# Kernel optimization log

Hardware: AMD Instinct MI355X
Metric: run time of the kernel (lower is better)

## Reference

```python
import jax, jax.numpy as jnp
import numpy as np
from jax import lax

BETA = 0.9
SLOPE = 25.0
THRESHOLD = 1.0
TIME_STEPS = 50


@jax.custom_vjp
def spike_fn(mem):
    # Heaviside fire: spk = 1 if mem > threshold
    return (mem > THRESHOLD).astype(mem.dtype)

def _spike_fwd(mem):
    return spike_fn(mem), mem

def _spike_bwd(mem, g):
    # snntorch fast_sigmoid surrogate: grad = 1 / (slope*|mem - thr| + 1)^2
    denom = SLOPE * jnp.abs(mem - THRESHOLD) + 1.0
    return (g / (denom * denom),)

spike_fn.defvjp(_spike_fwd, _spike_bwd)


def setup_inputs() -> dict:
    key = jax.random.key(0)
    k = jax.random.split(key, 5)
    B, D, H, O = 16384, 784, 128, 10
    return {
        "data": jax.random.normal(k[0], (B, D), dtype=jnp.float32),
        "W1": jax.random.normal(k[1], (H, D), dtype=jnp.float32) * (1.0 / np.sqrt(D)),
        "b1": jax.random.normal(k[2], (H,), dtype=jnp.float32) * 0.01,
        "W2": jax.random.normal(k[3], (O, H), dtype=jnp.float32) * (1.0 / np.sqrt(H)),
        "b2": jax.random.normal(k[4], (O,), dtype=jnp.float32) * 0.01,
    }


def reference(data, W1, b1, W2, b2):
    B = data.shape[0]
    H, O = W1.shape[0], W2.shape[0]
    # Input current to layer 1 is constant across time steps (static image).
    cur1 = data @ W1.T + b1  # [B, H]

    def step(carry, _):
        mem1, mem2 = carry
        # snntorch Leaky (reset_mechanism='subtract'):
        #   reset = detach(spk(mem_t)); mem_{t+1} = beta*mem_t + I - reset*thr; spk = fire(mem_{t+1})
        rst1 = lax.stop_gradient((mem1 > THRESHOLD).astype(mem1.dtype))
        mem1 = BETA * mem1 + cur1 - rst1 * THRESHOLD
        spk1 = spike_fn(mem1)

        cur2 = spk1 @ W2.T + b2  # [B, O]
        rst2 = lax.stop_gradient((mem2 > THRESHOLD).astype(mem2.dtype))
        mem2 = BETA * mem2 + cur2 - rst2 * THRESHOLD
        spk2 = spike_fn(mem2)
        return (mem1, mem2), spk2

    init = (jnp.zeros((B, H), data.dtype), jnp.zeros((B, O), data.dtype))
    _, spk_rec = lax.scan(step, init, None, length=TIME_STEPS)
    return spk_rec  # [time_steps, B, 10]
```

## Files before the change

kernel.cpp:

```cpp
#include <hip/hip_runtime.h>


#define TSTEPS 50
#define NB 16384
#define ND 784
#define NH 128
#define NO 10

#define BK 16
#define LDT 68

__global__ __launch_bounds__(256, 2)
void gemm_cur1(const float* __restrict__ data, const float* __restrict__ W1,
               const float* __restrict__ b1, float* __restrict__ cur1)
{
    __shared__ float As[BK * LDT];
    __shared__ float Ws[BK * LDT];

    const int tid  = threadIdx.x;
    const int bx   = blockIdx.x;
    const int bm   = bx >> 1;
    const int bn   = bx & 1;
    const int row0 = bm * 64;
    const int col0 = bn * 64;

    const int lm = tid >> 2;
    const int lk = (tid & 3) * 4;

    const float* aSrc = data + (size_t)(row0 + lm) * ND + lk;
    const float* wSrc = W1   + (size_t)(col0 + lm) * ND + lk;

    const int tx = tid & 15;
    const int ty = tid >> 4;

    float4 aReg = *(const float4*)aSrc;
    float4 wReg = *(const float4*)wSrc;

    float acc[4][4] = {};

    for (int c = 0; c < 49; ++c) {
        __syncthreads();
        As[(lk + 0) * LDT + lm] = aReg.x;
        As[(lk + 1) * LDT + lm] = aReg.y;
        As[(lk + 2) * LDT + lm] = aReg.z;
        As[(lk + 3) * LDT + lm] = aReg.w;
        Ws[(lk + 0) * LDT + lm] = wReg.x;
        Ws[(lk + 1) * LDT + lm] = wReg.y;
        Ws[(lk + 2) * LDT + lm] = wReg.z;
        Ws[(lk + 3) * LDT + lm] = wReg.w;
        __syncthreads();
        if (c < 48) {
            aReg = *(const float4*)(aSrc + (c + 1) * BK);
            wReg = *(const float4*)(wSrc + (c + 1) * BK);
        }
        #pragma unroll
        for (int k = 0; k < BK; ++k) {
            float4 a4 = *(const float4*)&As[k * LDT + ty * 4];
            float4 b4 = *(const float4*)&Ws[k * LDT + tx * 4];
            float av[4] = {a4.x, a4.y, a4.z, a4.w};
            float bv[4] = {b4.x, b4.y, b4.z, b4.w};
            #pragma unroll
            for (int i = 0; i < 4; ++i)
                #pragma unroll
                for (int j = 0; j < 4; ++j)
                    acc[i][j] = fmaf(av[i], bv[j], acc[i][j]);
        }
    }

    float4 bv1 = *(const float4*)&b1[col0 + tx * 4];
    #pragma unroll
    for (int i = 0; i < 4; ++i) {
        float4 o;
        o.x = acc[i][0] + bv1.x;
        o.y = acc[i][1] + bv1.y;
        o.z = acc[i][2] + bv1.z;
        o.w = acc[i][3] + bv1.w;
        *(float4*)&cur1[(size_t)(row0 + ty * 4 + i) * NH + col0 + tx * 4] = o;
    }
}

__global__ void snn_loop(const float* __restrict__ cur1,
                         const float* __restrict__ W2,
                         const float* __restrict__ b2,
                         float* __restrict__ out)
{
    const int tid = threadIdx.x;
    const int hg  = tid & 15;
    const int rl  = tid >> 4;
    const int row = blockIdx.x * 16 + rl;
    const int h0  = hg * 8;

    float w2[10][8];
    #pragma unroll
    for (int o = 0; o < 10; ++o) {
        float4 u = *(const float4*)&W2[o * NH + h0];
        float4 v = *(const float4*)&W2[o * NH + h0 + 4];
        w2[o][0] = u.x; w2[o][1] = u.y; w2[o][2] = u.z; w2[o][3] = u.w;
        w2[o][4] = v.x; w2[o][5] = v.y; w2[o][6] = v.z; w2[o][7] = v.w;
    }
    const float b2r = b2[hg < 10 ? hg : 0];

    float c[8];
    {
        float4 c0 = *(const float4*)&cur1[(size_t)row * NH + h0];
        float4 c1 = *(const float4*)&cur1[(size_t)row * NH + h0 + 4];
        c[0] = c0.x; c[1] = c0.y; c[2] = c0.z; c[3] = c0.w;
        c[4] = c1.x; c[5] = c1.y; c[6] = c1.z; c[7] = c1.w;
    }

    float mem1[8], spk1[8];
    #pragma unroll
    for (int j = 0; j < 8; ++j) { mem1[j] = 0.f; spk1[j] = 0.f; }
    float mem2 = 0.f, spk2 = 0.f;

    for (int t = 0; t < TSTEPS; ++t) {
        #pragma unroll
        for (int j = 0; j < 8; ++j) {
            float m = __fadd_rn(__fmul_rn(0.9f, mem1[j]), c[j]);
            m = __fsub_rn(m, spk1[j]);
            mem1[j] = m;
            spk1[j] = (m > 1.0f) ? 1.0f : 0.0f;
        }
        float p[10];
        #pragma unroll
        for (int o = 0; o < 10; ++o) p[o] = 0.f;
        #pragma unroll
        for (int j = 0; j < 8; ++j)
            #pragma unroll
            for (int o = 0; o < 10; ++o)
                p[o] = fmaf(spk1[j], w2[o][j], p[o]);
        #pragma unroll
        for (int m = 1; m <= 8; m <<= 1)
            #pragma unroll
            for (int o = 0; o < 10; ++o)
                p[o] += __shfl_xor(p[o], m, 64);
        float tot = p[0];
        #pragma unroll
        for (int o = 1; o < 10; ++o)
            tot = (hg == o) ? p[o] : tot;
        float cur2 = __fadd_rn(tot, b2r);
        float m2 = __fsub_rn(__fadd_rn(__fmul_rn(0.9f, mem2), cur2), spk2);
        mem2 = m2;
        spk2 = (m2 > 1.0f) ? 1.0f : 0.0f;
        if (hg < 10)
            out[(size_t)t * (NB * NO) + row * NO + hg] = spk2;
    }
}

extern "C" void kernel_launch(void* const* d_in, const int* in_sizes, int n_in,
                              void* d_out, int out_size, void* d_ws, size_t ws_size,
                              hipStream_t stream) {
    const float* data = (const float*)d_in[0];
    const float* W1   = (const float*)d_in[1];
    const float* b1   = (const float*)d_in[2];
    const float* W2   = (const float*)d_in[3];
    const float* b2   = (const float*)d_in[4];
    float* out  = (float*)d_out;
    float* cur1 = (float*)d_ws;

    gemm_cur1<<<512, 256, 0, stream>>>(data, W1, b1, cur1);
    snn_loop<<<1024, 256, 0, stream>>>(cur1, W2, b2, out);
}
```

Measured before the change: 230.0 us.

## Drop LDS staging in cur1 GEMM via transposed W1, use DPP reductions

Adds a kernel that transposes W1 into the workspace. The GEMM is rewritten to read operands directly from global memory into registers with one-step prefetch, so it no longer stages through shared memory or needs barriers. Separately, the cross-lane reduction in the SNN loop replaces __shfl_xor with DPP row moves and a ds_swizzle. This removes LDS traffic and shuffle overhead, but the GEMM now relies on cache for operand reuse and the extra launch adds latency.

Measured after the change: 252.4 us. 1.1x slower.

```diff
diff --git a/kernel.cpp b/kernel.cpp
--- a/kernel.cpp
+++ b/kernel.cpp
@@ -7,67 +7,77 @@
 #define NH 128
 #define NO 10
 
-#define BK 16
-#define LDT 68
+__global__ void w1_transpose(const float* __restrict__ W1, float* __restrict__ Wt)
+{
+    const int k = blockIdx.x;
+    const int n = threadIdx.x;
+    Wt[k * NH + n] = W1[n * ND + k];
+}
 
-__global__ __launch_bounds__(256, 2)
-void gemm_cur1(const float* __restrict__ data, const float* __restrict__ W1,
+__global__ __launch_bounds__(256)
+void gemm_cur1(const float* __restrict__ data, const float* __restrict__ Wt,
                const float* __restrict__ b1, float* __restrict__ cur1)
 {
-    __shared__ float As[BK * LDT];
-    __shared__ float Ws[BK * LDT];
-
     const int tid  = threadIdx.x;
-    const int bx   = blockIdx.x;
-    const int bm   = bx >> 1;
-    const int bn   = bx & 1;
+    const int bm   = blockIdx.x >> 1;
+    const int bn   = blockIdx.x & 1;
     const int row0 = bm * 64;
     const int col0 = bn * 64;
+    const int ty   = tid >> 4;
+    const int tn   = tid & 15;
 
-    const int lm = tid >> 2;
-    const int lk = (tid & 3) * 4;
-
-    const float* aSrc = data + (size_t)(row0 + lm) * ND + lk;
-    const float* wSrc = W1   + (size_t)(col0 + lm) * ND + lk;
-
-    const int tx = tid & 15;
-    const int ty = tid >> 4;
-
-    float4 aReg = *(const float4*)aSrc;
-    float4 wReg = *(const float4*)wSrc;
+    const float* aP0 = data + (size_t)(row0 + ty * 4 + 0) * ND;
+    const float* aP1 = data + (size_t)(row0 + ty * 4 + 1) * ND;
+    const float* aP2 = data + (size_t)(row0 + ty * 4 + 2) * ND;
+    const float* aP3 = data + (size_t)(row0 + ty * 4 + 3) * ND;
+    const float* bP  = Wt + col0 + tn * 4;
 
     float acc[4][4] = {};
 
-    for (int c = 0; c < 49; ++c) {
-        __syncthreads();
-        As[(lk + 0) * LDT + lm] = aReg.x;
-        As[(lk + 1) * LDT + lm] = aReg.y;
-        As[(lk + 2) * LDT + lm] = aReg.z;
-        As[(lk + 3) * LDT + lm] = aReg.w;
-        Ws[(lk + 0) * LDT + lm] = wReg.x;
-        Ws[(lk + 1) * LDT + lm] = wReg.y;
-        Ws[(lk + 2) * LDT + lm] = wReg.z;
-        Ws[(lk + 3) * LDT + lm] = wReg.w;
-        __syncthreads();
-        if (c < 48) {
-            aReg = *(const float4*)(aSrc + (c + 1) * BK);
-            wReg = *(const float4*)(wSrc + (c + 1) * BK);
+    float4 aCur[4], bCur[4];
+    aCur[0] = *(const float4*)(aP0);
+    aCur[1] = *(const float4*)(aP1);
+    aCur[2] = *(const float4*)(aP2);
+    aCur[3] = *(const float4*)(aP3);
+    bCur[0] = *(const float4*)(bP + 0 * NH);
+    bCur[1] = *(const float4*)(bP + 1 * NH);
+    bCur[2] = *(const float4*)(bP + 2 * NH);
+    bCur[3] = *(const float4*)(bP + 3 * NH);
+
+    for (int c = 0; c < 196; ++c) {
+        float4 aNxt[4], bNxt[4];
+        if (c < 195) {
+            const int k4 = (c + 1) * 4;
+            aNxt[0] = *(const float4*)(aP0 + k4);
+            aNxt[1] = *(const float4*)(aP1 + k4);
+            aNxt[2] = *(const float4*)(aP2 + k4);
+            aNxt[3] = *(const float4*)(aP3 + k4);
+            bNxt[0] = *(const float4*)(bP + (size_t)(k4 + 0) * NH);
+            bNxt[1] = *(const float4*)(bP + (size_t)(k4 + 1) * NH);
+            bNxt[2] = *(const float4*)(bP + (size_t)(k4 + 2) * NH);
+            bNxt[3] = *(const float4*)(bP + (size_t)(k4 + 3) * NH);
         }
         #pragma unroll
-        for (int k = 0; k < BK; ++k) {
-            float4 a4 = *(const float4*)&As[k * LDT + ty * 4];
-            float4 b4 = *(const float4*)&Ws[k * LDT + tx * 4];
-            float av[4] = {a4.x, a4.y, a4.z, a4.w};
-            float bv[4] = {b4.x, b4.y, b4.z, b4.w};
+        for (int kk = 0; kk < 4; ++kk) {
+            float a[4] = { ((const float*)&aCur[0])[kk],
+                           ((const float*)&aCur[1])[kk],
+                           ((const float*)&aCur[2])[kk],
+                           ((const float*)&aCur[3])[kk] };
+            float b[4] = { ((const float*)&bCur[kk])[0],
+                           ((const float*)&bCur[kk])[1],
+                           ((const float*)&bCur[kk])[2],
+                           ((const float*)&bCur[kk])[3] };
             #pragma unroll
             for (int i = 0; i < 4; ++i)
                 #pragma unroll
                 for (int j = 0; j < 4; ++j)
-                    acc[i][j] = fmaf(av[i], bv[j], acc[i][j]);
+                    acc[i][j] = fmaf(a[i], b[j], acc[i][j]);
         }
+        #pragma unroll
+        for (int q = 0; q < 4; ++q) { aCur[q] = aNxt[q]; bCur[q] = bNxt[q]; }
     }
 
-    float4 bv1 = *(const float4*)&b1[col0 + tx * 4];
+    float4 bv1 = *(const float4*)&b1[col0 + tn * 4];
     #pragma unroll
     for (int i = 0; i < 4; ++i) {
         float4 o;
@@ -75,8 +85,25 @@
         o.y = acc[i][1] + bv1.y;
         o.z = acc[i][2] + bv1.z;
         o.w = acc[i][3] + bv1.w;
-        *(float4*)&cur1[(size_t)(row0 + ty * 4 + i) * NH + col0 + tx * 4] = o;
+        *(float4*)&cur1[(size_t)(row0 + ty * 4 + i) * NH + col0 + tn * 4] = o;
     }
+}
+
+__device__ __forceinline__ float xmove_dpp_b1(float v) {
+    return __int_as_float(__builtin_amdgcn_update_dpp(
+        0, __float_as_int(v), 0xB1, 0xF, 0xF, true));
+}
+__device__ __forceinline__ float xmove_dpp_b2(float v) {
+    return __int_as_float(__builtin_amdgcn_update_dpp(
+        0, __float_as_int(v), 0x4E, 0xF, 0xF, true));
+}
+__device__ __forceinline__ float xmove_dpp_b8(float v) {
+    return __int_as_float(__builtin_amdgcn_update_dpp(
+        0, __float_as_int(v), 0x128, 0xF, 0xF, true));
+}
+__device__ __forceinline__ float xmove_swz_b4(float v) {
+    return __int_as_float(__builtin_amdgcn_ds_swizzle(
+        __float_as_int(v), 0x101F));
 }
 
 __global__ void snn_loop(const float* __restrict__ cur1,
@@ -130,10 +157,13 @@
             for (int o = 0; o < 10; ++o)
                 p[o] = fmaf(spk1[j], w2[o][j], p[o]);
         #pragma unroll
-        for (int m = 1; m <= 8; m <<= 1)
-            #pragma unroll
-            for (int o = 0; o < 10; ++o)
-                p[o] += __shfl_xor(p[o], m, 64);
+        for (int o = 0; o < 10; ++o) p[o] += xmove_dpp_b1(p[o]);
+        #pragma unroll
+        for (int o = 0; o < 10; ++o) p[o] += xmove_dpp_b2(p[o]);
+        #pragma unroll
+        for (int o = 0; o < 10; ++o) p[o] += xmove_swz_b4(p[o]);
+        #pragma unroll
+        for (int o = 0; o < 10; ++o) p[o] += xmove_dpp_b8(p[o]);
         float tot = p[0];
         #pragma unroll
         for (int o = 1; o < 10; ++o)
@@ -156,8 +186,11 @@
     const float* W2   = (const float*)d_in[3];
     const float* b2   = (const float*)d_in[4];
     float* out  = (float*)d_out;
+
     float* cur1 = (float*)d_ws;
+    float* Wt   = (float*)((char*)d_ws + (size_t)NB * NH * 4);
 
-    gemm_cur1<<<512, 256, 0, stream>>>(data, W1, b1, cur1);
+    w1_transpose<<<ND, NH, 0, stream>>>(W1, Wt);
+    gemm_cur1<<<512, 256, 0, stream>>>(data, Wt, b1, cur1);
     snn_loop<<<1024, 256, 0, stream>>>(cur1, W2, b2, out);
 }
```
